# Kernel tuning notes

Measured on AMD Instinct MI355X. Metric: run time of the kernel, lower is better.

Reference implementation:

```python
import jax, jax.numpy as jnp
import numpy as np

TOP_K = 8


def setup_inputs() -> dict:
    key = jax.random.key(0)
    ks = jax.random.split(key, 8)
    B, S, H, BD, N, VBD = 4, 2048, 2048, 256, 256, 256
    return {
        "hidden_states": jax.random.normal(ks[0], (B, S, H), jnp.float32),
        "primary_attention_output": jax.random.normal(ks[1], (B, S, H), jnp.float32),
        "q_proj_w": jax.random.normal(ks[2], (BD, H), jnp.float32) / np.sqrt(H),
        "slot_keys": jax.random.normal(ks[3], (N, BD), jnp.float32),
        "slot_values": jax.random.normal(ks[4], (N, H), jnp.float32),
        "reliability": jax.random.uniform(ks[5], (N,), jnp.float32, 1e-3, 1.0),
        "value_down_w": jax.random.normal(ks[6], (VBD, H), jnp.float32) * 0.1 / np.sqrt(H),
        "value_up_w": jax.random.normal(ks[7], (H, VBD), jnp.float32) * 0.1 / np.sqrt(VBD),
    }


def reference(hidden_states, primary_attention_output, q_proj_w, slot_keys,
              slot_values, reliability, value_down_w, value_up_w):
    B, S, H = hidden_states.shape
    BD = q_proj_w.shape[0]
    # query = q_proj(hidden_states): [B,S,BD]
    query = jnp.einsum("bsh,dh->bsd", hidden_states, q_proj_w)
    # gate-chain scoring: query . slot_keys scaled, plus log-reliability mask
    rel_mask = jnp.log(jnp.clip(reliability, 1e-10))            # [N]
    scores = jnp.einsum("bsd,nd->bsn", query, slot_keys) / jnp.sqrt(
        jnp.asarray(BD, query.dtype)) + rel_mask                # [B,S,N]
    top_scores, top_idx = jax.lax.top_k(scores, TOP_K)          # [B,S,K]
    attn = jax.nn.softmax(top_scores, axis=-1)                  # [B,S,K]
    final_gate = jax.nn.sigmoid(top_scores[..., 0])             # [B,S]
    # slot-pool gather + weighted sum of values (irregular access)
    vals = slot_values[top_idx]                                 # [B,S,K,H]
    aux = jnp.einsum("bsk,bskh->bsh", attn, vals)               # [B,S,H]
    # low-rank value projection with GELU
    aux = jnp.einsum("bsh,vh->bsv", aux, value_down_w)
    aux = jax.nn.gelu(aux)
    aux = jnp.einsum("bsv,hv->bsh", aux, value_up_w)
    return primary_attention_output + final_gate[..., None] * aux
```

## Files before the change

### kernel.cpp

```cpp
#include <hip/hip_runtime.h>
#include <stdint.h>


typedef float f32x4 __attribute__((ext_vector_type(4)));
typedef unsigned short u16x8 __attribute__((ext_vector_type(8)));
typedef unsigned short u16x4 __attribute__((ext_vector_type(4)));
typedef __bf16 bf16x8 __attribute__((ext_vector_type(8)));

#define WS_QW    0u
#define WS_SK    1048576u
#define WS_SV    1179648u
#define WS_VDW   2228224u
#define WS_VUP   3276800u
#define WS_REL   4325376u
#define WS_PV    4326400u
#define WS_GATE  4588544u
#define WS_QP    4621312u
#define WS_D     21398528u

static __device__ __forceinline__ unsigned short f2bf(float f) {
  union { float f; unsigned int u; } v; v.f = f;
  unsigned int r = v.u + 0x7FFFu + ((v.u >> 16) & 1u);
  return (unsigned short)(r >> 16);
}
static __device__ __forceinline__ bf16x8 as_bf16(u16x8 v) {
  return __builtin_bit_cast(bf16x8, v);
}
static __device__ __forceinline__ float gelu_tanh(float x) {
  float u = 0.7978845608028654f * (x + 0.044715f * x * x * x);
  return 0.5f * x * (1.0f + tanhf(u));
}

__global__ void k_prep(const float* __restrict__ qw, const float* __restrict__ sk,
                       const float* __restrict__ sv, const float* __restrict__ vdw,
                       const float* __restrict__ vup, const float* __restrict__ rel,
                       unsigned char* __restrict__ ws) {
  unsigned short* o_qw  = (unsigned short*)(ws + WS_QW);
  unsigned short* o_sk  = (unsigned short*)(ws + WS_SK);
  unsigned short* o_sv  = (unsigned short*)(ws + WS_SV);
  unsigned short* o_vdw = (unsigned short*)(ws + WS_VDW);
  unsigned short* o_vup = (unsigned short*)(ws + WS_VUP);
  float* o_rel = (float*)(ws + WS_REL);
  int tid = blockIdx.x * blockDim.x + threadIdx.x;
  int stride = gridDim.x * blockDim.x;
  for (int g = tid; g < 540736; g += stride) {
    const float* src; unsigned short* dst; int i;
    if      (g < 131072) { src = qw;  dst = o_qw;  i = g; }
    else if (g < 147456) { src = sk;  dst = o_sk;  i = g - 131072; }
    else if (g < 278528) { src = sv;  dst = o_sv;  i = g - 147456; }
    else if (g < 409600) { src = vdw; dst = o_vdw; i = g - 278528; }
    else if (g < 540672) { src = vup; dst = o_vup; i = g - 409600; }
    else {
      int i4 = (g - 540672) * 4;
      #pragma unroll
      for (int j = 0; j < 4; j++) o_rel[i4 + j] = logf(fmaxf(rel[i4 + j], 1e-10f));
      continue;
    }
    f32x4 v = *(const f32x4*)(src + (size_t)i * 4);
    u16x4 o;
    #pragma unroll
    for (int j = 0; j < 4; j++) o[j] = f2bf(v[j]);
    *(u16x4*)(dst + (size_t)i * 4) = o;
  }
}

__global__ __launch_bounds__(256, 2) void k_pv(unsigned char* __restrict__ ws) {
  const unsigned short* sv  = (const unsigned short*)(ws + WS_SV);
  const unsigned short* vdw = (const unsigned short*)(ws + WS_VDW);
  float* PV = (float*)(ws + WS_PV);
  __shared__ __align__(16) unsigned short As[32 * 64];
  __shared__ __align__(16) unsigned short Bs[32 * 64];
  int t = threadIdx.x, lane = t & 63, w = t >> 6;
  int nt = blockIdx.x >> 3, vt = blockIdx.x & 7;
  int mf = w >> 1, nf = w & 1;
  f32x4 acc = {0.f, 0.f, 0.f, 0.f};
  int r = t >> 3, c = t & 7;
  int sw8 = (c ^ (r & 7)) * 8;
  for (int k0 = 0; k0 < 2048; k0 += 64) {
    __syncthreads();
    *(u16x8*)&As[r * 64 + sw8] = *(const u16x8*)&sv[(size_t)(nt * 32 + r) * 2048 + k0 + c * 8];
    *(u16x8*)&Bs[r * 64 + sw8] = *(const u16x8*)&vdw[(size_t)(vt * 32 + r) * 2048 + k0 + c * 8];
    __syncthreads();
    #pragma unroll
    for (int kk = 0; kk < 2; kk++) {
      int ck = kk * 4 + (lane >> 4);
      int ar = mf * 16 + (lane & 15);
      int br = nf * 16 + (lane & 15);
      bf16x8 a = as_bf16(*(const u16x8*)&As[ar * 64 + ((ck ^ (ar & 7)) * 8)]);
      bf16x8 b = as_bf16(*(const u16x8*)&Bs[br * 64 + ((ck ^ (br & 7)) * 8)]);
      acc = __builtin_amdgcn_mfma_f32_16x16x32_bf16(a, b, acc, 0, 0, 0);
    }
  }
  int row = nt * 32 + mf * 16 + (lane >> 4) * 4;
  int col = vt * 32 + nf * 16 + (lane & 15);
  #pragma unroll
  for (int j = 0; j < 4; j++) PV[(row + j) * 256 + col] = acc[j];
}

__global__ __launch_bounds__(256, 4) void k_query(const float* __restrict__ hs,
                                                  unsigned char* __restrict__ ws) {
  const unsigned short* qw = (const unsigned short*)(ws + WS_QW);
  float* qp = (float*)(ws + WS_QP);
  __shared__ __align__(16) unsigned short As[32 * 64];
  __shared__ __align__(16) unsigned short Bs[256 * 64];
  int t = threadIdx.x, lane = t & 63, w = t >> 6;
  int rt = blockIdx.x >> 1, ks = blockIdx.x & 1;
  int row0 = rt * 32, kbase = ks * 1024;
  f32x4 acc[2][4] = {};
  int sr = t >> 3, sc = t & 7;
  const float* aptr = hs + (size_t)(row0 + sr) * 2048 + kbase + sc * 8;
  const unsigned short* bptr = qw + (size_t)sr * 2048 + kbase + sc * 8;
  f32x4 pa0, pa1;
  u16x8 pb0, pb1, pb2, pb3, pb4, pb5, pb6, pb7;
  pa0 = *(const f32x4*)(aptr);
  pa1 = *(const f32x4*)(aptr + 4);
  pb0 = *(const u16x8*)(bptr + (size_t)0 * 32 * 2048);
  pb1 = *(const u16x8*)(bptr + (size_t)1 * 32 * 2048);
  pb2 = *(const u16x8*)(bptr + (size_t)2 * 32 * 2048);
  pb3 = *(const u16x8*)(bptr + (size_t)3 * 32 * 2048);
  pb4 = *(const u16x8*)(bptr + (size_t)4 * 32 * 2048);
  pb5 = *(const u16x8*)(bptr + (size_t)5 * 32 * 2048);
  pb6 = *(const u16x8*)(bptr + (size_t)6 * 32 * 2048);
  pb7 = *(const u16x8*)(bptr + (size_t)7 * 32 * 2048);
  for (int kt = 0; kt < 16; kt++) {
    __syncthreads();
    {
      u16x8 o;
      #pragma unroll
      for (int j = 0; j < 4; j++) { o[j] = f2bf(pa0[j]); o[4 + j] = f2bf(pa1[j]); }
      *(u16x8*)&As[sr * 64 + ((sc ^ (sr & 7)) * 8)] = o;
      u16x8 pb[8] = {pb0, pb1, pb2, pb3, pb4, pb5, pb6, pb7};
      #pragma unroll
      for (int i = 0; i < 8; i++) {
        int n = i * 32 + sr;
        *(u16x8*)&Bs[n * 64 + ((sc ^ (n & 7)) * 8)] = pb[i];
      }
    }
    __syncthreads();
    if (kt < 15) {
      int off = (kt + 1) * 64;
      pa0 = *(const f32x4*)(aptr + off);
      pa1 = *(const f32x4*)(aptr + off + 4);
      pb0 = *(const u16x8*)(bptr + (size_t)0 * 32 * 2048 + off);
      pb1 = *(const u16x8*)(bptr + (size_t)1 * 32 * 2048 + off);
      pb2 = *(const u16x8*)(bptr + (size_t)2 * 32 * 2048 + off);
      pb3 = *(const u16x8*)(bptr + (size_t)3 * 32 * 2048 + off);
      pb4 = *(const u16x8*)(bptr + (size_t)4 * 32 * 2048 + off);
      pb5 = *(const u16x8*)(bptr + (size_t)5 * 32 * 2048 + off);
      pb6 = *(const u16x8*)(bptr + (size_t)6 * 32 * 2048 + off);
      pb7 = *(const u16x8*)(bptr + (size_t)7 * 32 * 2048 + off);
    }
    #pragma unroll
    for (int kk = 0; kk < 2; kk++) {
      int ck = kk * 4 + (lane >> 4);
      bf16x8 a[2], b[4];
      #pragma unroll
      for (int mf = 0; mf < 2; mf++) {
        int arow = mf * 16 + (lane & 15);
        a[mf] = as_bf16(*(const u16x8*)&As[arow * 64 + ((ck ^ (arow & 7)) * 8)]);
      }
      #pragma unroll
      for (int nf = 0; nf < 4; nf++) {
        int brow = w * 64 + nf * 16 + (lane & 15);
        b[nf] = as_bf16(*(const u16x8*)&Bs[brow * 64 + ((ck ^ (brow & 7)) * 8)]);
      }
      #pragma unroll
      for (int mf = 0; mf < 2; mf++)
        #pragma unroll
        for (int nf = 0; nf < 4; nf++)
          acc[mf][nf] = __builtin_amdgcn_mfma_f32_16x16x32_bf16(a[mf], b[nf], acc[mf][nf], 0, 0, 0);
    }
  }
  float* outp = qp + (size_t)ks * 8192 * 256;
  #pragma unroll
  for (int mf = 0; mf < 2; mf++) {
    int row = row0 + mf * 16 + (lane >> 4) * 4;
    #pragma unroll
    for (int nf = 0; nf < 4; nf++) {
      int col = w * 64 + nf * 16 + (lane & 15);
      #pragma unroll
      for (int j = 0; j < 4; j++) outp[(size_t)(row + j) * 256 + col] = acc[mf][nf][j];
    }
  }
}

#define QSTR 264
#define SSTR 260
__global__ __launch_bounds__(256, 4) void k_score(unsigned char* __restrict__ ws) {
  const float* qp = (const float*)(ws + WS_QP);
  const unsigned short* sk = (const unsigned short*)(ws + WS_SK);
  const float* relm = (const float*)(ws + WS_REL);
  const float* PV = (const float*)(ws + WS_PV);
  float* gates = (float*)(ws + WS_GATE);
  unsigned short* D = (unsigned short*)(ws + WS_D);
  __shared__ __align__(16) unsigned short Qs[16 * QSTR];
  __shared__ __align__(16) float Ss[16 * SSTR];
  int t = threadIdx.x, lane = t & 63, w = t >> 6;
  int row0 = blockIdx.x * 16;
  #pragma unroll
  for (int i = 0; i < 4; i++) {
    int id = i * 256 + t, r = id >> 6, c4 = id & 63;
    const float* p0 = qp + (size_t)(row0 + r) * 256 + c4 * 4;
    f32x4 a = *(const f32x4*)p0;
    f32x4 b = *(const f32x4*)(p0 + 8192 * 256);
    u16x4 o;
    #pragma unroll
    for (int j = 0; j < 4; j++) o[j] = f2bf(a[j] + b[j]);
    *(u16x4*)&Qs[r * QSTR + c4 * 4] = o;
  }
  __syncthreads();
  {
    f32x4 acc[4] = {};
    for (int ksb = 0; ksb < 8; ksb++) {
      int ck = lane >> 4;
      bf16x8 a = as_bf16(*(const u16x8*)&Qs[(lane & 15) * QSTR + ksb * 32 + ck * 8]);
      #pragma unroll
      for (int nf = 0; nf < 4; nf++) {
        int n = w * 64 + nf * 16 + (lane & 15);
        bf16x8 b = as_bf16(*(const u16x8*)&sk[(size_t)n * 256 + ksb * 32 + ck * 8]);
        acc[nf] = __builtin_amdgcn_mfma_f32_16x16x32_bf16(a, b, acc[nf], 0, 0, 0);
      }
    }
    #pragma unroll
    for (int nf = 0; nf < 4; nf++) {
      int n = w * 64 + nf * 16 + (lane & 15);
      float rm = relm[n];
      int rr = (lane >> 4) * 4;
      #pragma unroll
      for (int j = 0; j < 4; j++) Ss[(rr + j) * SSTR + n] = acc[nf][j] * 0.0625f + rm;
    }
  }
  __syncthreads();
  for (int rr = 0; rr < 4; rr++) {
    int row = w * 4 + rr;
    f32x4 sv4 = *(const f32x4*)&Ss[row * SSTR + lane * 4];
    unsigned int key[4];
    #pragma unroll
    for (int j = 0; j < 4; j++) {
      unsigned int u = __builtin_bit_cast(unsigned int, sv4[j]);
      unsigned int os = (u & 0x80000000u) ? ~u : (u | 0x80000000u);
      key[j] = (os & 0xFFFFFF00u) | (unsigned int)(255 - (lane * 4 + j));
    }
    unsigned int win[8];
    #pragma unroll
    for (int e = 0; e < 8; e++) {
      unsigned int m01 = key[0] > key[1] ? key[0] : key[1];
      unsigned int m23 = key[2] > key[3] ? key[2] : key[3];
      unsigned int m = m01 > m23 ? m01 : m23;
      #pragma unroll
      for (int d = 1; d < 64; d <<= 1) {
        unsigned int o = (unsigned int)__shfl_xor((int)m, d, 64);
        m = o > m ? o : m;
      }
      win[e] = m;
      #pragma unroll
      for (int j = 0; j < 4; j++) if (key[j] == m) key[j] = 0u;
    }
    float s8[8]; int i8[8];
    #pragma unroll
    for (int e = 0; e < 8; e++) {
      i8[e] = 255 - (int)(win[e] & 0xFFu);
      unsigned int os = win[e] & 0xFFFFFF00u;
      unsigned int u = (os & 0x80000000u) ? (os ^ 0x80000000u) : ~os;
      s8[e] = __builtin_bit_cast(float, u);
    }
    float m0 = s8[0], sum = 0.f, we[8];
    #pragma unroll
    for (int e = 0; e < 8; e++) { we[e] = expf(s8[e] - m0); sum += we[e]; }
    float inv = 1.f / sum;
    f32x4 accv = {0.f, 0.f, 0.f, 0.f};
    #pragma unroll
    for (int e = 0; e < 8; e++) {
      float wk = we[e] * inv;
      f32x4 p = *(const f32x4*)(PV + (size_t)i8[e] * 256 + lane * 4);
      #pragma unroll
      for (int j = 0; j < 4; j++) accv[j] += wk * p[j];
    }
    u16x4 o;
    #pragma unroll
    for (int j = 0; j < 4; j++) o[j] = f2bf(gelu_tanh(accv[j]));
    *(u16x4*)&D[(size_t)(row0 + row) * 256 + lane * 4] = o;
    if (lane == 0) gates[row0 + row] = 1.f / (1.f + expf(-m0));
  }
}

union KOutLds {
  unsigned short AB[2][128 * 64];
  float stage[32 * 132];
};
__global__ __launch_bounds__(256, 4) void k_out(const float* __restrict__ primary,
                                                float* __restrict__ out,
                                                unsigned char* __restrict__ ws) {
  const unsigned short* D = (const unsigned short*)(ws + WS_D);
  const unsigned short* vup = (const unsigned short*)(ws + WS_VUP);
  const float* gates = (const float*)(ws + WS_GATE);
  __shared__ __align__(16) KOutLds u;
  __shared__ float gate_s[128];
  unsigned short* As = u.AB[0];
  unsigned short* Bs = u.AB[1];
  int t = threadIdx.x, lane = t & 63, w = t >> 6;
  int bid = blockIdx.x;
  int L = (bid & 7) * 128 + (bid >> 3);
  int rt = L >> 4, ct = L & 15;
  int wm = w >> 1, wn = w & 1;
  f32x4 acc[4][4] = {};
  if (t < 128) gate_s[t] = gates[rt * 128 + t];
  for (int k0 = 0; k0 < 256; k0 += 64) {
    __syncthreads();
    #pragma unroll
    for (int i = 0; i < 4; i++) {
      int id = i * 256 + t, r = id >> 3, c = id & 7;
      int sw8 = (c ^ (r & 7)) * 8;
      *(u16x8*)&As[r * 64 + sw8] = *(const u16x8*)&D[(size_t)(rt * 128 + r) * 256 + k0 + c * 8];
      *(u16x8*)&Bs[r * 64 + sw8] = *(const u16x8*)&vup[(size_t)(ct * 128 + r) * 256 + k0 + c * 8];
    }
    __syncthreads();
    #pragma unroll
    for (int kk = 0; kk < 2; kk++) {
      int ck = kk * 4 + (lane >> 4);
      bf16x8 a[4], b[4];
      #pragma unroll
      for (int mf = 0; mf < 4; mf++) {
        int ar = wm * 64 + mf * 16 + (lane & 15);
        a[mf] = as_bf16(*(const u16x8*)&As[ar * 64 + ((ck ^ (ar & 7)) * 8)]);
      }
      #pragma unroll
      for (int nf = 0; nf < 4; nf++) {
        int br = wn * 64 + nf * 16 + (lane & 15);
        b[nf] = as_bf16(*(const u16x8*)&Bs[br * 64 + ((ck ^ (br & 7)) * 8)]);
      }
      #pragma unroll
      for (int mf = 0; mf < 4; mf++)
        #pragma unroll
        for (int nf = 0; nf < 4; nf++)
          acc[mf][nf] = __builtin_amdgcn_mfma_f32_16x16x32_bf16(a[mf], b[nf], acc[mf][nf], 0, 0, 0);
    }
  }
  #pragma unroll
  for (int c = 0; c < 4; c++) {
    __syncthreads();
    if (wm == (c >> 1)) {
      #pragma unroll
      for (int mi = 0; mi < 2; mi++) {
        int mf = (c & 1) * 2 + mi;
        #pragma unroll
        for (int nf = 0; nf < 4; nf++) {
          int col = wn * 64 + nf * 16 + (lane & 15);
          #pragma unroll
          for (int j = 0; j < 4; j++) {
            int r = mi * 16 + (lane >> 4) * 4 + j;
            u.stage[r * 132 + col] = acc[mf][nf][j];
          }
        }
      }
    }
    __syncthreads();
    #pragma unroll
    for (int i = 0; i < 4; i++) {
      int idx = i * 256 + t, r = idx >> 5, c4 = idx & 31;
      int row = rt * 128 + c * 32 + r;
      size_t o = (size_t)row * 2048 + ct * 128 + c4 * 4;
      f32x4 p = *(const f32x4*)(primary + o);
      f32x4 s = *(const f32x4*)&u.stage[r * 132 + c4 * 4];
      float g = gate_s[c * 32 + r];
      f32x4 ov;
      #pragma unroll
      for (int j = 0; j < 4; j++) ov[j] = p[j] + g * s[j];
      *(f32x4*)(out + o) = ov;
    }
  }
}

extern "C" void kernel_launch(void* const* d_in, const int* in_sizes, int n_in,
                              void* d_out, int out_size, void* d_ws, size_t ws_size,
                              hipStream_t stream) {
  const float* hs      = (const float*)d_in[0];
  const float* primary = (const float*)d_in[1];
  const float* qw      = (const float*)d_in[2];
  const float* sk      = (const float*)d_in[3];
  const float* sv      = (const float*)d_in[4];
  const float* rel     = (const float*)d_in[5];
  const float* vdw     = (const float*)d_in[6];
  const float* vup     = (const float*)d_in[7];
  unsigned char* ws = (unsigned char*)d_ws;
  float* out = (float*)d_out;

  k_prep<<<dim3(256), dim3(256), 0, stream>>>(qw, sk, sv, vdw, vup, rel, ws);
  k_pv<<<dim3(64), dim3(256), 0, stream>>>(ws);
  k_query<<<dim3(512), dim3(256), 0, stream>>>(hs, ws);
  k_score<<<dim3(512), dim3(256), 0, stream>>>(ws);
  k_out<<<dim3(1024), dim3(256), 0, stream>>>(primary, out, ws);
}
```

Measured before the change: 96.24 us.

## Restructure k_out GEMM to keep full-K B tile in LDS with register-prefetched A

The output GEMM kernel now loads a 64-column slice of value_up_w across the full K=256 into swizzled LDS once per block. Each wave then streams its A rows (the D activations) directly from global memory into registers, double-buffering them along with the primary-output and gate values across four row tiles. This removes the per-k-step block-wide barriers and the shared A tile, and gives each wave a private staging buffer for the epilogue instead of block-synchronized staging. In exchange, register pressure rises (occupancy hint drops from 4 to 3) and A fragments are read uncoalesced from global memory with no reuse across waves.

```diff
diff --git a/kernel.cpp b/kernel.cpp
--- a/kernel.cpp
+++ b/kernel.cpp
@@ -284,89 +284,82 @@
   }
 }
 
-union KOutLds {
-  unsigned short AB[2][128 * 64];
-  float stage[32 * 132];
-};
-__global__ __launch_bounds__(256, 4) void k_out(const float* __restrict__ primary,
+__global__ __launch_bounds__(256, 3) void k_out(const float* __restrict__ primary,
                                                 float* __restrict__ out,
                                                 unsigned char* __restrict__ ws) {
   const unsigned short* D = (const unsigned short*)(ws + WS_D);
   const unsigned short* vup = (const unsigned short*)(ws + WS_VUP);
   const float* gates = (const float*)(ws + WS_GATE);
-  __shared__ __align__(16) KOutLds u;
-  __shared__ float gate_s[128];
-  unsigned short* As = u.AB[0];
-  unsigned short* Bs = u.AB[1];
+  __shared__ __align__(16) unsigned short Bs[64 * 256];
+  __shared__ __align__(16) float stage[4][16 * 68];
   int t = threadIdx.x, lane = t & 63, w = t >> 6;
   int bid = blockIdx.x;
   int L = (bid & 7) * 128 + (bid >> 3);
-  int rt = L >> 4, ct = L & 15;
-  int wm = w >> 1, wn = w & 1;
-  f32x4 acc[4][4] = {};
-  if (t < 128) gate_s[t] = gates[rt * 128 + t];
-  for (int k0 = 0; k0 < 256; k0 += 64) {
-    __syncthreads();
-    #pragma unroll
-    for (int i = 0; i < 4; i++) {
-      int id = i * 256 + t, r = id >> 3, c = id & 7;
-      int sw8 = (c ^ (r & 7)) * 8;
-      *(u16x8*)&As[r * 64 + sw8] = *(const u16x8*)&D[(size_t)(rt * 128 + r) * 256 + k0 + c * 8];
-      *(u16x8*)&Bs[r * 64 + sw8] = *(const u16x8*)&vup[(size_t)(ct * 128 + r) * 256 + k0 + c * 8];
-    }
-    __syncthreads();
-    #pragma unroll
-    for (int kk = 0; kk < 2; kk++) {
-      int ck = kk * 4 + (lane >> 4);
-      bf16x8 a[4], b[4];
-      #pragma unroll
-      for (int mf = 0; mf < 4; mf++) {
-        int ar = wm * 64 + mf * 16 + (lane & 15);
-        a[mf] = as_bf16(*(const u16x8*)&As[ar * 64 + ((ck ^ (ar & 7)) * 8)]);
-      }
+  int g = L >> 5, ct = L & 31;
+  #pragma unroll
+  for (int it = 0; it < 8; it++) {
+    int id = it * 256 + t, n = id >> 5, c = id & 31;
+    int cs = (c & 24) | ((c & 7) ^ (n & 7));
+    *(u16x8*)&Bs[n * 256 + cs * 8] =
+        *(const u16x8*)&vup[(size_t)(ct * 64 + n) * 256 + c * 8];
+  }
+  int row0 = g * 256 + w * 16;
+  const unsigned short* aLane = D + (size_t)(row0 + (lane & 15)) * 256 + (lane >> 4) * 8;
+  const float* pPtr = primary + (size_t)(row0 + (lane >> 4)) * 2048 + ct * 64 + (lane & 15) * 4;
+  float* oPtr = out + (size_t)(row0 + (lane >> 4)) * 2048 + ct * 64 + (lane & 15) * 4;
+  const float* gPtr = gates + row0 + (lane >> 4);
+  u16x8 a[2][8];
+  f32x4 p[2][4];
+  float gt[2][4];
+  #pragma unroll
+  for (int kb = 0; kb < 8; kb++) a[0][kb] = *(const u16x8*)(aLane + kb * 32);
+  #pragma unroll
+  for (int it = 0; it < 4; it++) {
+    p[0][it] = *(const f32x4*)(pPtr + (size_t)it * 4 * 2048);
+    gt[0][it] = gPtr[it * 4];
+  }
+  __syncthreads();
+  float* st = &stage[w][0];
+  #pragma unroll
+  for (int rt = 0; rt < 4; rt++) {
+    int cur = rt & 1;
+    if (rt < 3) {
+      #pragma unroll
+      for (int kb = 0; kb < 8; kb++)
+        a[cur ^ 1][kb] = *(const u16x8*)(aLane + (size_t)(rt + 1) * 64 * 256 + kb * 32);
+      #pragma unroll
+      for (int it = 0; it < 4; it++) {
+        p[cur ^ 1][it] = *(const f32x4*)(pPtr + (size_t)((rt + 1) * 64 + it * 4) * 2048);
+        gt[cur ^ 1][it] = gPtr[(rt + 1) * 64 + it * 4];
+      }
+    }
+    f32x4 acc[4] = {};
+    #pragma unroll
+    for (int kb = 0; kb < 8; kb++) {
+      bf16x8 av = as_bf16(a[cur][kb]);
       #pragma unroll
       for (int nf = 0; nf < 4; nf++) {
-        int br = wn * 64 + nf * 16 + (lane & 15);
-        b[nf] = as_bf16(*(const u16x8*)&Bs[br * 64 + ((ck ^ (br & 7)) * 8)]);
-      }
-      #pragma unroll
-      for (int mf = 0; mf < 4; mf++)
-        #pragma unroll
-        for (int nf = 0; nf < 4; nf++)
-          acc[mf][nf] = __builtin_amdgcn_mfma_f32_16x16x32_bf16(a[mf], b[nf], acc[mf][nf], 0, 0, 0);
-    }
-  }
-  #pragma unroll
-  for (int c = 0; c < 4; c++) {
-    __syncthreads();
-    if (wm == (c >> 1)) {
-      #pragma unroll
-      for (int mi = 0; mi < 2; mi++) {
-        int mf = (c & 1) * 2 + mi;
-        #pragma unroll
-        for (int nf = 0; nf < 4; nf++) {
-          int col = wn * 64 + nf * 16 + (lane & 15);
-          #pragma unroll
-          for (int j = 0; j < 4; j++) {
-            int r = mi * 16 + (lane >> 4) * 4 + j;
-            u.stage[r * 132 + col] = acc[mf][nf][j];
-          }
-        }
-      }
-    }
-    __syncthreads();
-    #pragma unroll
-    for (int i = 0; i < 4; i++) {
-      int idx = i * 256 + t, r = idx >> 5, c4 = idx & 31;
-      int row = rt * 128 + c * 32 + r;
-      size_t o = (size_t)row * 2048 + ct * 128 + c4 * 4;
-      f32x4 p = *(const f32x4*)(primary + o);
-      f32x4 s = *(const f32x4*)&u.stage[r * 132 + c4 * 4];
-      float g = gate_s[c * 32 + r];
+        int n = nf * 16 + (lane & 15);
+        int c = kb * 4 + (lane >> 4);
+        int cs = (c & 24) | ((c & 7) ^ (n & 7));
+        bf16x8 bv = as_bf16(*(const u16x8*)&Bs[n * 256 + cs * 8]);
+        acc[nf] = __builtin_amdgcn_mfma_f32_16x16x32_bf16(av, bv, acc[nf], 0, 0, 0);
+      }
+    }
+    #pragma unroll
+    for (int nf = 0; nf < 4; nf++)
+      #pragma unroll
+      for (int j = 0; j < 4; j++)
+        st[((lane >> 4) * 4 + j) * 68 + nf * 16 + (lane & 15)] = acc[nf][j];
+    #pragma unroll
+    for (int it = 0; it < 4; it++) {
+      f32x4 s = *(const f32x4*)&st[(it * 4 + (lane >> 4)) * 68 + (lane & 15) * 4];
+      f32x4 pv = p[cur][it];
+      float gv = gt[cur][it];
       f32x4 ov;
       #pragma unroll
-      for (int j = 0; j < 4; j++) ov[j] = p[j] + g * s[j];
-      *(f32x4*)(out + o) = ov;
+      for (int j = 0; j < 4; j++) ov[j] = pv[j] + gv * s[j];
+      *(f32x4*)(oPtr + (size_t)(rt * 64 + it * 4) * 2048) = ov;
     }
   }
 }
```

Measured after the change: 97.79 us. About the same (+1.6%).
